# Optimization experiments

Measured on AMD Instinct MI355X. Metric: run time of the kernel, lower is better.

Reference implementation:

```python
import jax, jax.numpy as jnp
import numpy as np

THR = 0.5
IOU_THR = 0.2
K = 4096          # fixed pre-NMS candidate budget (jit-compatible stand-in for thr filtering + full sort)
FEAT_OFF = 5      # cols: 0 obj score, 1:5 box (l,t,r,b), 5: class-feature embedding


def setup_inputs() -> dict:
    key = jax.random.key(0)
    kx, kl, kt, kw, kh, ks, kp, kr = jax.random.split(key, 8)
    C, H, W = 261, 320, 320  # 5 + 256 feature channels
    x = jax.random.normal(kx, (1, C, H, W), dtype=jnp.float32)
    # plausible (l,t,r,b) boxes in padded-image coordinates so NMS has real work
    l = jax.random.uniform(kl, (1, 1, H, W), dtype=jnp.float32) * 600.0
    t = jax.random.uniform(kt, (1, 1, H, W), dtype=jnp.float32) * 600.0
    r = l + jax.random.uniform(kw, (1, 1, H, W), dtype=jnp.float32) * 60.0
    b = t + jax.random.uniform(kh, (1, 1, H, W), dtype=jnp.float32) * 60.0
    x = x.at[:, 1:5].set(jnp.concatenate([l, t, r, b], axis=1))
    state_matrix = jax.random.normal(ks, (16, 256), dtype=jnp.float32)
    padding = jax.random.uniform(kp, (2,), dtype=jnp.float32) * 10.0
    ratio = jax.random.uniform(kr, (1,), dtype=jnp.float32) * 0.6 + 0.4
    return {"x": x, "state_matrix": state_matrix, "padding": padding,
            "ratio": ratio, "image_width": 1280, "image_height": 768}


def _pairwise_iou(boxes, eps=1e-10):
    # boxes: [K, 4] as (l, t, r, b); returns [K, K]
    l, t, r, b = boxes[:, 0], boxes[:, 1], boxes[:, 2], boxes[:, 3]
    area = (r - l) * (b - t)
    iw = jnp.clip(jnp.minimum(r[:, None], r[None, :]) - jnp.maximum(l[:, None], l[None, :]), 0.0)
    ih = jnp.clip(jnp.minimum(b[:, None], b[None, :]) - jnp.maximum(t[:, None], t[None, :]), 0.0)
    inter = iw * ih
    union = area[:, None] + area[None, :] - inter + eps
    return inter / union


def reference(x, state_matrix, padding, ratio, image_width, image_height):
    B, C, H, W = x.shape
    out = x[0].reshape(C, H * W).T                      # [N, C]
    sig = jax.nn.sigmoid(out[:, 0])                     # sigmoid on objectness channel
    cls_logits = out[:, FEAT_OFF:] @ state_matrix.T     # [N, 16] class-state matmul
    cls_val = jnp.max(cls_logits, axis=1)
    cls_idx = jnp.argmax(cls_logits, axis=1)
    score = sig * cls_val                               # out[:,0] * cls_values
    valid = sig > THR                                   # out[0] > thr filter
    score = jnp.where(valid, score, -jnp.inf)
    topv, topi = jax.lax.top_k(score, K)                # descending sort, fixed budget
    boxes = out[topi, 1:5]                              # [K, 4] (l,t,r,b)
    cls_k = cls_idx[topi]
    area = (boxes[:, 2] - boxes[:, 0]) * (boxes[:, 3] - boxes[:, 1])
    iou = _pairwise_iou(boxes)                          # [K, K]

    alive0 = jnp.isfinite(topv)                         # only thr-passing candidates enter the queue
    kept0 = jnp.zeros((K,), dtype=bool)

    def body(carry, i):
        alive, kept = carry
        is_cur = alive[i]                               # still in the queue (not suppressed earlier)
        alive = alive.at[i].set(False)                  # pop top
        ious_i = iou[i]
        n_over = jnp.sum((ious_i >= IOU_THR) & alive)   # remaining boxes with iou >= thr
        accept = is_cur & (area[i] >= 4.0) & (n_over >= 10)
        kept = kept.at[i].set(accept)
        alive = jnp.where(accept, alive & (ious_i < IOU_THR), alive)  # suppress only on accept
        return (alive, kept), None

    (_, kept), _ = jax.lax.scan(body, (alive0, kept0), jnp.arange(K))

    keep = kept & (topv >= THR)                         # p[0,0] < thr -> skip
    inv_r = 1.0 / ratio[0]
    x1 = jnp.maximum((boxes[:, 0] - padding[0]) * inv_r, 0.0)
    y1 = jnp.maximum((boxes[:, 1] - padding[1]) * inv_r, 0.0)
    x2 = jnp.minimum((boxes[:, 2] - padding[0]) * inv_r, jnp.float32(image_width))
    y2 = jnp.minimum((boxes[:, 3] - padding[1]) * inv_r, jnp.float32(image_height))
    keep = keep & (x1 < image_width) & (y1 < image_height)

    dets = jnp.stack([jnp.ones((K,), jnp.float32), topv, x1, y1, x2, y2,
                      cls_k.astype(jnp.float32)], axis=1)   # [K, 7]
    dets = jnp.where(keep[:, None], dets, 0.0)
    return dets
```

## Files before the change

kernel.cpp:

```cpp
#include <hip/hip_runtime.h>
#include <hip/hip_bf16.h>
#include <math.h>

#define HW 102400
#define KSEL 4096
#define CAP 16384

__device__ inline unsigned fkey(float f) {
    unsigned u = __float_as_uint(f);
    return (u & 0x80000000u) ? ~u : (u | 0x80000000u);
}

__device__ inline unsigned wave_sum64_s(unsigned x) {
    x += (unsigned)__builtin_amdgcn_update_dpp(0, (int)x, 0x111, 0xf, 0xf, false);
    x += (unsigned)__builtin_amdgcn_update_dpp(0, (int)x, 0x112, 0xf, 0xf, false);
    x += (unsigned)__builtin_amdgcn_update_dpp(0, (int)x, 0x114, 0xf, 0xf, false);
    x += (unsigned)__builtin_amdgcn_update_dpp(0, (int)x, 0x118, 0xf, 0xf, false);
    x += (unsigned)__builtin_amdgcn_update_dpp(0, (int)x, 0x142, 0xa, 0xf, false);
    x += (unsigned)__builtin_amdgcn_update_dpp(0, (int)x, 0x143, 0xc, 0xf, false);
    return (unsigned)__builtin_amdgcn_readlane((int)x, 63);
}

__device__ inline unsigned long long readlane64(unsigned long long v, int l) {
    unsigned lo = (unsigned)__builtin_amdgcn_readlane((int)(unsigned)(v & 0xffffffffull), l);
    unsigned hi = (unsigned)__builtin_amdgcn_readlane((int)(unsigned)(v >> 32), l);
    return ((unsigned long long)hi << 32) | lo;
}

__global__ __launch_bounds__(256) void k_score(const float* __restrict__ x,
                                               const float* __restrict__ sm,
                                               float* __restrict__ score,
                                               int* __restrict__ clsidx) {
    __shared__ float swt[256][16];
    __shared__ float tile[2][16][256];
    int t = threadIdx.x;
    for (int i = t; i < 4096; i += 256) {
        int k = i >> 8, c = i & 255;
        swt[c][k] = sm[i];
    }
    int wave = t >> 6, lane = t & 63;
    size_t pxb = (size_t)blockIdx.x * 256;
    const float* xc = x + (size_t)5 * HW + pxb;

    float acc[16];
#pragma unroll
    for (int k = 0; k < 16; ++k) acc[k] = 0.f;

    float4 sa[4], sb[4];

#define LOADX(dst, ti)                                                         \
    _Pragma("unroll") for (int j = 0; j < 4; ++j)                              \
        dst[j] = *(const float4*)(xc + (size_t)((ti) * 16 + wave * 4 + j) * HW + lane * 4);
#define STOREX(src, s)                                                         \
    _Pragma("unroll") for (int j = 0; j < 4; ++j)                              \
        ((float4*)&tile[s][wave * 4 + j][0])[lane] = src[j];
#define COMP(s, ti)                                                            \
    _Pragma("unroll") for (int cc = 0; cc < 16; ++cc) {                        \
        float xv = tile[s][cc][t];                                             \
        const float4* w4 = (const float4*)&swt[(ti) * 16 + cc][0];             \
        float4 w0 = w4[0], w1 = w4[1], w2 = w4[2], w3 = w4[3];                 \
        acc[0]  = fmaf(xv, w0.x, acc[0]);  acc[1]  = fmaf(xv, w0.y, acc[1]);   \
        acc[2]  = fmaf(xv, w0.z, acc[2]);  acc[3]  = fmaf(xv, w0.w, acc[3]);   \
        acc[4]  = fmaf(xv, w1.x, acc[4]);  acc[5]  = fmaf(xv, w1.y, acc[5]);   \
        acc[6]  = fmaf(xv, w1.z, acc[6]);  acc[7]  = fmaf(xv, w1.w, acc[7]);   \
        acc[8]  = fmaf(xv, w2.x, acc[8]);  acc[9]  = fmaf(xv, w2.y, acc[9]);   \
        acc[10] = fmaf(xv, w2.z, acc[10]); acc[11] = fmaf(xv, w2.w, acc[11]);  \
        acc[12] = fmaf(xv, w3.x, acc[12]); acc[13] = fmaf(xv, w3.y, acc[13]);  \
        acc[14] = fmaf(xv, w3.z, acc[14]); acc[15] = fmaf(xv, w3.w, acc[15]);  \
    }

    LOADX(sa, 0);
    STOREX(sa, 0);
    LOADX(sa, 1);
    LOADX(sb, 2);
    __syncthreads();

#pragma unroll
    for (int k = 0; k < 16; k += 2) {
        COMP(k & 1, k);
        STOREX(sa, (k + 1) & 1);
        if (k + 3 < 16) LOADX(sa, k + 3);
        __syncthreads();
        COMP((k + 1) & 1, k + 1);
        if (k + 2 < 16) { STOREX(sb, k & 1); }
        if (k + 4 < 16) LOADX(sb, k + 4);
        __syncthreads();
    }
#undef LOADX
#undef STOREX
#undef COMP

    float mv = acc[0]; int mi = 0;
#pragma unroll
    for (int k = 1; k < 16; ++k)
        if (acc[k] > mv) { mv = acc[k]; mi = k; }
    int n = (int)pxb + t;
    float x0 = x[n];
    float sig = 1.0f / (1.0f + expf(-x0));
    float sc = (sig > 0.5f) ? sig * mv : -INFINITY;
    score[n] = sc;
    clsidx[n] = mi;
}

__global__ void k_hist(const float* __restrict__ score, unsigned* __restrict__ hist) {
    int n = blockIdx.x * 256 + threadIdx.x;
    float sc = score[n];
    if (sc != -INFINITY) atomicAdd(&hist[fkey(sc) >> 16], 1u);
}

__global__ __launch_bounds__(1024) void k_findp(const unsigned* __restrict__ hist,
                                                unsigned* __restrict__ meta) {
    __shared__ unsigned part[1024];
    __shared__ unsigned sgrp, s_after;
    __shared__ unsigned bins[64];
    int t = threadIdx.x;
    if (t == 0) { sgrp = 0; s_after = 0; }
    unsigned s = 0;
    const unsigned* hp = hist + t * 64;
    for (int i = 0; i < 64; ++i) s += hp[i];
    part[t] = s;
    __syncthreads();
    for (int off = 1; off < 1024; off <<= 1) {
        unsigned v = (t + off < 1024) ? part[t + off] : 0u;
        __syncthreads();
        part[t] += v;
        __syncthreads();
    }
    if (part[t] >= KSEL && (t == 1023 || part[t + 1] < KSEL)) {
        sgrp = (unsigned)t;
        s_after = (t == 1023) ? 0u : part[t + 1];
    }
    __syncthreads();
    unsigned g = sgrp, SA = s_after;
    if (t < 64) bins[t] = hist[g * 64 + t];
    __syncthreads();
    if (t == 0) {
        unsigned acc = SA, p = g * 64;
        for (int b = 63; b >= 0; --b) {
            acc += bins[b];
            if (acc >= KSEL) { p = g * 64 + (unsigned)b; break; }
        }
        meta[1] = p;
    }
}

__global__ void k_collect(const float* __restrict__ score,
                          unsigned* __restrict__ meta,
                          unsigned long long* __restrict__ cand) {
    int n = blockIdx.x * 256 + threadIdx.x;
    unsigned key = fkey(score[n]);
    if ((key >> 16) >= meta[1]) {
        unsigned pos = atomicAdd(&meta[0], 1u);
        if (pos < CAP)
            cand[pos] = ((unsigned long long)key << 32) | (unsigned)(~(unsigned)n);
    }
}

__global__ __launch_bounds__(256) void k_rank(const unsigned long long* __restrict__ cand,
                                              const unsigned* __restrict__ meta,
                                              const float* __restrict__ x,
                                              const float* __restrict__ score,
                                              const int* __restrict__ clsidx,
                                              float* __restrict__ topv,
                                              float* __restrict__ bl, float* __restrict__ bt,
                                              float* __restrict__ br, float* __restrict__ bb,
                                              float* __restrict__ area, int* __restrict__ clsk) {
    __shared__ unsigned long long tile[1024];
    int C = (int)meta[0]; if (C > CAP) C = CAP;
    int j = blockIdx.x * 256 + threadIdx.x;
    unsigned long long kj = (j < C) ? cand[j] : 0ull;
    unsigned rank = 0;
    for (int tb = 0; tb < C; tb += 1024) {
        int cnt = min(1024, C - tb);
        __syncthreads();
        for (int u = threadIdx.x; u < cnt; u += 256) tile[u] = cand[tb + u];
        __syncthreads();
        if (j < C)
            for (int u = 0; u < cnt; ++u) rank += (tile[u] > kj) ? 1u : 0u;
    }
    if (j < C && rank < KSEL) {
        unsigned n = ~(unsigned)(kj & 0xFFFFFFFFull);
        float l  = x[(size_t)1 * HW + n];
        float tt = x[(size_t)2 * HW + n];
        float r  = x[(size_t)3 * HW + n];
        float b  = x[(size_t)4 * HW + n];
        topv[rank] = score[n];
        bl[rank] = l; bt[rank] = tt; br[rank] = r; bb[rank] = b;
        area[rank] = (r - l) * (b - tt);
        clsk[rank] = clsidx[n];
    }
}

__global__ __launch_bounds__(256) void k_mask(const float* __restrict__ bl, const float* __restrict__ bt,
                                              const float* __restrict__ br, const float* __restrict__ bb,
                                              const float* __restrict__ area,
                                              unsigned long long* __restrict__ mask) {
    __shared__ float sl[256], st[256], sr[256], sb[256], sa[256];
    int t = threadIdx.x;
    int ic = blockIdx.x >> 4;
    int jc = blockIdx.x & 15;
    int i = ic * 256 + t;
    int j0 = jc * 256;
    sl[t] = bl[j0 + t]; st[t] = bt[j0 + t]; sr[t] = br[j0 + t];
    sb[t] = bb[j0 + t]; sa[t] = area[j0 + t];
    __syncthreads();
    float li = bl[i], ti = bt[i], ri = br[i], bi = bb[i], ai = area[i];
#pragma unroll
    for (int w = 0; w < 4; ++w) {
        unsigned long long m = 0;
        for (int k2 = 0; k2 < 64; ++k2) {
            int j = w * 64 + k2;
            float iw = fminf(ri, sr[j]) - fmaxf(li, sl[j]); iw = fmaxf(iw, 0.f);
            float ih = fminf(bi, sb[j]) - fmaxf(ti, st[j]); ih = fmaxf(ih, 0.f);
            float inter = iw * ih;
            float uni = ai + sa[j] - inter + 1e-10f;
            if (inter / uni >= 0.2f) m |= (1ull << k2);
        }
        mask[(size_t)i * 64 + (jc * 4 + w)] = m;
    }
}

__global__ __launch_bounds__(64, 1) void k_nms(const unsigned long long* __restrict__ mask,
                                               const float* __restrict__ topv,
                                               const float* __restrict__ area,
                                               unsigned long long* __restrict__ keptW) {
    __shared__ unsigned long long rowsL[2][4096];
    int lane = threadIdx.x;

#define STAGE(bb, s)                                                            \
    do {                                                                        \
        _Pragma("unroll") for (int q = 0; q < 32; ++q) {                        \
            int r_ = (bb) * 64 + q * 2 + (lane >> 5);                           \
            int P_ = (lane & 31) ^ (r_ & 31);                                   \
            const unsigned long long* gp_ = mask + (size_t)r_ * 64 + P_ * 2;    \
            __builtin_amdgcn_global_load_lds(                                   \
                (const __attribute__((address_space(1))) void*)gp_,             \
                (__attribute__((address_space(3))) void*)&rowsL[s][q * 128],    \
                16, 0, 0);                                                      \
        }                                                                       \
    } while (0)

    STAGE(0, 0);
    STAGE(1, 1);

    unsigned long long alive = 0, areaok = 0;
    for (int k = 0; k < 64; ++k) {
        float tv = topv[(size_t)k * 64 + lane];
        float ar = area[(size_t)k * 64 + lane];
        unsigned long long b1 = __ballot(tv != -INFINITY);
        unsigned long long b2 = __ballot(ar >= 4.0f);
        if (lane == k) { alive = b1; areaok = b2; }
    }

    for (int b = 0; b < 64; ++b) {
        if (b < 63) {
            asm volatile("s_waitcnt vmcnt(32)" ::: "memory");
        } else {
            asm volatile("s_waitcnt vmcnt(0)" ::: "memory");
        }
        __builtin_amdgcn_sched_barrier(0);

        const unsigned long long* rb = rowsL[b & 1];
        unsigned long long aw0snap = readlane64(alive, b);
        unsigned long long areaok0 = readlane64(areaok, b);

        int sw = lane & 31;
        unsigned cnt = 0;
#pragma unroll
        for (int P = 0; P < 32; ++P) {
            const ulonglong2 rv = *(const ulonglong2*)&rb[lane * 64 + ((P ^ sw) << 1)];
            unsigned long long a0 = readlane64(alive, 2 * P);
            unsigned long long a1 = readlane64(alive, 2 * P + 1);
            cnt += (unsigned)__popcll(rv.x & a0) + (unsigned)__popcll(rv.y & a1);
        }
        unsigned long long m_w0 = rb[lane * 64 + ((((b >> 1) ^ sw)) << 1) + (b & 1)];
        unsigned long long pfx = (lane == 63) ? ~0ull : ((1ull << (lane + 1)) - 1ull);
        cnt -= (unsigned)__popcll(m_w0 & aw0snap & pfx);

        bool candp = (cnt >= 10u) && ((areaok0 >> lane) & 1ull) && ((aw0snap >> lane) & 1ull);
        unsigned long long cand = __ballot(candp);
        unsigned long long keptB = 0;

        while (cand) {
            int j1 = __ffsll(cand) - 1;
            cand &= cand - 1;
            unsigned long long aw0cur = readlane64(alive, b);
            if (!((aw0cur >> j1) & 1ull)) continue;
            unsigned long long rw = rb[(size_t)j1 * 64 + (((lane >> 1) ^ (j1 & 31)) << 1) + (lane & 1)];
            unsigned long long awAdj = alive;
            unsigned long long pm = (j1 == 63) ? ~0ull : ((1ull << (j1 + 1)) - 1ull);
            if (lane == b) awAdj &= ~pm;
            unsigned c = (unsigned)__popcll(rw & awAdj);
            unsigned tt = wave_sum64_s(c);
            if (tt >= 10u) {
                alive &= ~rw;
                keptB |= 1ull << j1;
            }
        }

        if (lane == b) alive = 0;
        if (lane == 0) keptW[b] = keptB;

        if (b + 2 < 64) { STAGE(b + 2, (b & 1)); }
    }
#undef STAGE
}

__global__ __launch_bounds__(256) void k_out(const unsigned long long* __restrict__ keptW,
                                             const float* __restrict__ topv,
                                             const float* __restrict__ bl, const float* __restrict__ bt,
                                             const float* __restrict__ br, const float* __restrict__ bb,
                                             const int* __restrict__ clsk,
                                             const float* __restrict__ padding,
                                             const float* __restrict__ ratio,
                                             const int* __restrict__ piw, const int* __restrict__ pih,
                                             float* __restrict__ out) {
    int i = blockIdx.x * 256 + threadIdx.x;
    if (i >= KSEL) return;
    bool kept = (keptW[i >> 6] >> (i & 63)) & 1ull;
    float tv = topv[i];
    bool keep = kept && (tv >= 0.5f);
    float p0 = padding[0], p1 = padding[1];
    float invr = 1.0f / ratio[0];
    float W_ = (float)piw[0], H_ = (float)pih[0];
    float x1 = fmaxf((bl[i] - p0) * invr, 0.f);
    float y1 = fmaxf((bt[i] - p1) * invr, 0.f);
    float x2 = fminf((br[i] - p0) * invr, W_);
    float y2 = fminf((bb[i] - p1) * invr, H_);
    keep = keep && (x1 < W_) && (y1 < H_);
    float* o = out + (size_t)i * 7;
    if (keep) {
        o[0] = 1.0f; o[1] = tv; o[2] = x1; o[3] = y1; o[4] = x2; o[5] = y2;
        o[6] = (float)clsk[i];
    } else {
        o[0] = 0.f; o[1] = 0.f; o[2] = 0.f; o[3] = 0.f; o[4] = 0.f; o[5] = 0.f; o[6] = 0.f;
    }
}

extern "C" void kernel_launch(void* const* d_in, const int* in_sizes, int n_in,
                              void* d_out, int out_size, void* d_ws, size_t ws_size,
                              hipStream_t stream) {
    const float* x       = (const float*)d_in[0];
    const float* sm      = (const float*)d_in[1];
    const float* padding = (const float*)d_in[2];
    const float* ratio   = (const float*)d_in[3];
    const int*   piw     = (const int*)d_in[4];
    const int*   pih     = (const int*)d_in[5];
    float* out = (float*)d_out;
    char* ws = (char*)d_ws;

    float* score               = (float*)(ws + 0);
    int*   clsidx              = (int*)(ws + 409600);
    unsigned* hist             = (unsigned*)(ws + 819200);
    unsigned* meta             = (unsigned*)(ws + 1081344);
    unsigned long long* cand   = (unsigned long long*)(ws + 1081856);
    float* topv                = (float*)(ws + 1212928);
    float* bl                  = (float*)(ws + 1229312);
    float* bt                  = (float*)(ws + 1245696);
    float* br                  = (float*)(ws + 1262080);
    float* bb                  = (float*)(ws + 1278464);
    float* area                = (float*)(ws + 1294848);
    int*   clsk                = (int*)(ws + 1311232);
    unsigned long long* keptW  = (unsigned long long*)(ws + 1327616);
    unsigned long long* mask   = (unsigned long long*)(ws + 1328128);

    hipMemsetAsync(hist, 0, 262144 + 512, stream);

    k_score  <<<400, 256, 0, stream>>>(x, sm, score, clsidx);
    k_hist   <<<400, 256, 0, stream>>>(score, hist);
    k_findp  <<<1, 1024, 0, stream>>>(hist, meta);
    k_collect<<<400, 256, 0, stream>>>(score, meta, cand);
    k_rank   <<<CAP / 256, 256, 0, stream>>>(cand, meta, x, score, clsidx,
                                             topv, bl, bt, br, bb, area, clsk);
    k_mask   <<<256, 256, 0, stream>>>(bl, bt, br, bb, area, mask);
    k_nms    <<<1, 64, 0, stream>>>(mask, topv, area, keptW);
    k_out    <<<16, 256, 0, stream>>>(keptW, topv, bl, bt, br, bb, clsk,
                                      padding, ratio, piw, pih, out);
}
```

Measured before the change: 374.7 us.

## Split NMS block counting across four waves with LDS alive mask and batched verify

The serial NMS kernel goes from one wave to four. All four waves compute the per-row overlap counts in parallel: each row's 64 words are split over 4 threads, combined with DPP, and read against an alive mask broadcast through LDS. Wave 0 alone runs the sequential accept loop, preloading up to four candidate rows per iteration to hide LDS latency. Row staging moves to a rotated layout spread across waves. The price is three block barriers per 64-row block in a latency-bound single-block kernel.

```diff
diff --git a/kernel.cpp b/kernel.cpp
--- a/kernel.cpp
+++ b/kernel.cpp
@@ -220,22 +220,43 @@
     }
 }
 
-__global__ __launch_bounds__(64, 1) void k_nms(const unsigned long long* __restrict__ mask,
-                                               const float* __restrict__ topv,
-                                               const float* __restrict__ area,
-                                               unsigned long long* __restrict__ keptW) {
+__global__ __launch_bounds__(256, 1) void k_nms(const unsigned long long* __restrict__ mask,
+                                                const float* __restrict__ topv,
+                                                const float* __restrict__ area,
+                                                unsigned long long* __restrict__ keptW) {
     __shared__ unsigned long long rowsL[2][4096];
-    int lane = threadIdx.x;
+    __shared__ unsigned long long aliveL[64];
+    __shared__ unsigned cntL[64];
+    int t = threadIdx.x;
+    int lane = t & 63;
+    int W = t >> 6;
+    int g = t & 3;
+    int jrow = t >> 2;
+
+    unsigned long long alive = 0, areaok = 0, keptAcc = 0;
+    if (W == 0) {
+        for (int k = 0; k < 64; ++k) {
+            float tv = topv[(size_t)k * 64 + lane];
+            float ar = area[(size_t)k * 64 + lane];
+            unsigned long long b1 = __ballot(tv != -INFINITY);
+            unsigned long long b2 = __ballot(ar >= 4.0f);
+            if (lane == k) { alive = b1; areaok = b2; }
+        }
+        aliveL[lane] = alive;
+    }
 
 #define STAGE(bb, s)                                                            \
     do {                                                                        \
-        _Pragma("unroll") for (int q = 0; q < 32; ++q) {                        \
-            int r_ = (bb) * 64 + q * 2 + (lane >> 5);                           \
-            int P_ = (lane & 31) ^ (r_ & 31);                                   \
-            const unsigned long long* gp_ = mask + (size_t)r_ * 64 + P_ * 2;    \
+        _Pragma("unroll") for (int i = 0; i < 8; ++i) {                         \
+            int seg_ = i * 4 + W;                                               \
+            int r_ = seg_ * 2 + (lane >> 5);                                    \
+            int p_ = (lane & 31) * 2;                                           \
+            int wl_ = (p_ - 2 * r_) & 63;                                       \
+            const unsigned long long* gp_ =                                     \
+                mask + ((size_t)((bb) * 64 + r_) * 64 + wl_);                   \
             __builtin_amdgcn_global_load_lds(                                   \
                 (const __attribute__((address_space(1))) void*)gp_,             \
-                (__attribute__((address_space(3))) void*)&rowsL[s][q * 128],    \
+                (__attribute__((address_space(3))) void*)&rowsL[s][seg_ * 128], \
                 16, 0, 0);                                                      \
         }                                                                       \
     } while (0)
@@ -243,67 +264,82 @@
     STAGE(0, 0);
     STAGE(1, 1);
 
-    unsigned long long alive = 0, areaok = 0;
-    for (int k = 0; k < 64; ++k) {
-        float tv = topv[(size_t)k * 64 + lane];
-        float ar = area[(size_t)k * 64 + lane];
-        unsigned long long b1 = __ballot(tv != -INFINITY);
-        unsigned long long b2 = __ballot(ar >= 4.0f);
-        if (lane == k) { alive = b1; areaok = b2; }
+#define VER(jj, rw)                                                             \
+    {                                                                           \
+        unsigned long long awc = readlane64(alive, b);                          \
+        if ((awc >> (jj)) & 1ull) {                                             \
+            unsigned long long awAdj = alive;                                   \
+            unsigned long long pm = ((jj) == 63) ? ~0ull                        \
+                                                 : ((1ull << ((jj) + 1)) - 1ull); \
+            if (lane == b) awAdj &= ~pm;                                        \
+            unsigned c_ = (unsigned)__popcll((rw) & awAdj);                     \
+            unsigned tt_ = wave_sum64_s(c_);                                    \
+            if (tt_ >= 10u) { alive &= ~(rw); keptB |= 1ull << (jj); }          \
+        }                                                                       \
     }
 
     for (int b = 0; b < 64; ++b) {
-        if (b < 63) {
-            asm volatile("s_waitcnt vmcnt(32)" ::: "memory");
-        } else {
-            asm volatile("s_waitcnt vmcnt(0)" ::: "memory");
-        }
+        if (b < 63) asm volatile("s_waitcnt vmcnt(8)" ::: "memory");
+        else        asm volatile("s_waitcnt vmcnt(0)" ::: "memory");
         __builtin_amdgcn_sched_barrier(0);
-
-        const unsigned long long* rb = rowsL[b & 1];
-        unsigned long long aw0snap = readlane64(alive, b);
-        unsigned long long areaok0 = readlane64(areaok, b);
-
-        int sw = lane & 31;
+        __builtin_amdgcn_s_barrier();
+
+        const unsigned long long* rb = &rowsL[b & 1][0];
+
+        unsigned long long pfxj = (jrow == 63) ? ~0ull : ((1ull << (jrow + 1)) - 1ull);
+        int base_w = g * 16;
         unsigned cnt = 0;
 #pragma unroll
-        for (int P = 0; P < 32; ++P) {
-            const ulonglong2 rv = *(const ulonglong2*)&rb[lane * 64 + ((P ^ sw) << 1)];
-            unsigned long long a0 = readlane64(alive, 2 * P);
-            unsigned long long a1 = readlane64(alive, 2 * P + 1);
-            cnt += (unsigned)__popcll(rv.x & a0) + (unsigned)__popcll(rv.y & a1);
+        for (int q = 0; q < 8; ++q) {
+            int wl = base_w + q * 2;
+            int ph = (wl + 2 * jrow) & 63;
+            ulonglong2 rv = *(const ulonglong2*)&rb[jrow * 64 + ph];
+            ulonglong2 av = *(const ulonglong2*)&aliveL[wl];
+            unsigned cx = (unsigned)__popcll(rv.x & av.x);
+            unsigned cy = (unsigned)__popcll(rv.y & av.y);
+            cnt += cx + cy;
+            if (wl == b)     cnt -= (unsigned)__popcll(rv.x & av.x & pfxj);
+            if (wl + 1 == b) cnt -= (unsigned)__popcll(rv.y & av.y & pfxj);
         }
-        unsigned long long m_w0 = rb[lane * 64 + ((((b >> 1) ^ sw)) << 1) + (b & 1)];
-        unsigned long long pfx = (lane == 63) ? ~0ull : ((1ull << (lane + 1)) - 1ull);
-        cnt -= (unsigned)__popcll(m_w0 & aw0snap & pfx);
-
-        bool candp = (cnt >= 10u) && ((areaok0 >> lane) & 1ull) && ((aw0snap >> lane) & 1ull);
-        unsigned long long cand = __ballot(candp);
-        unsigned long long keptB = 0;
-
-        while (cand) {
-            int j1 = __ffsll(cand) - 1;
-            cand &= cand - 1;
-            unsigned long long aw0cur = readlane64(alive, b);
-            if (!((aw0cur >> j1) & 1ull)) continue;
-            unsigned long long rw = rb[(size_t)j1 * 64 + (((lane >> 1) ^ (j1 & 31)) << 1) + (lane & 1)];
-            unsigned long long awAdj = alive;
-            unsigned long long pm = (j1 == 63) ? ~0ull : ((1ull << (j1 + 1)) - 1ull);
-            if (lane == b) awAdj &= ~pm;
-            unsigned c = (unsigned)__popcll(rw & awAdj);
-            unsigned tt = wave_sum64_s(c);
-            if (tt >= 10u) {
-                alive &= ~rw;
-                keptB |= 1ull << j1;
+        cnt += (unsigned)__builtin_amdgcn_update_dpp(0, (int)cnt, 0xB1, 0xf, 0xf, false);
+        cnt += (unsigned)__builtin_amdgcn_update_dpp(0, (int)cnt, 0x4E, 0xf, 0xf, false);
+        if (g == 0) cntL[jrow] = cnt;
+        asm volatile("s_waitcnt lgkmcnt(0)" ::: "memory");
+        __builtin_amdgcn_s_barrier();
+
+        if (W == 0) {
+            unsigned long long keptB = 0;
+            unsigned long long aw0snap = readlane64(alive, b);
+            unsigned long long areaok0 = readlane64(areaok, b);
+            unsigned myc = cntL[lane];
+            bool candp = (myc >= 10u) && ((areaok0 >> lane) & 1ull) &&
+                         ((aw0snap >> lane) & 1ull);
+            unsigned long long cand = __ballot(candp);
+            while (cand) {
+                int j1 = __ffsll(cand) - 1; cand &= cand - 1;
+                int j2 = -1, j3 = -1, j4 = -1;
+                if (cand) { j2 = __ffsll(cand) - 1; cand &= cand - 1; }
+                if (cand) { j3 = __ffsll(cand) - 1; cand &= cand - 1; }
+                if (cand) { j4 = __ffsll(cand) - 1; cand &= cand - 1; }
+                unsigned long long r1 = rb[j1 * 64 + ((lane + 2 * j1) & 63)];
+                unsigned long long r2 = (j2 >= 0) ? rb[j2 * 64 + ((lane + 2 * j2) & 63)] : 0;
+                unsigned long long r3 = (j3 >= 0) ? rb[j3 * 64 + ((lane + 2 * j3) & 63)] : 0;
+                unsigned long long r4 = (j4 >= 0) ? rb[j4 * 64 + ((lane + 2 * j4) & 63)] : 0;
+                VER(j1, r1);
+                if (j2 >= 0) VER(j2, r2);
+                if (j3 >= 0) VER(j3, r3);
+                if (j4 >= 0) VER(j4, r4);
             }
+            if (lane == b) { alive = 0; keptAcc = keptB; }
+            aliveL[lane] = alive;
         }
-
-        if (lane == b) alive = 0;
-        if (lane == 0) keptW[b] = keptB;
-
-        if (b + 2 < 64) { STAGE(b + 2, (b & 1)); }
-    }
+        asm volatile("s_waitcnt lgkmcnt(0)" ::: "memory");
+        __builtin_amdgcn_s_barrier();
+        if (b + 2 < 64) STAGE(b + 2, b & 1);
+    }
+    if (W == 0) keptW[lane] = keptAcc;
 #undef STAGE
+#undef VER
 }
 
 __global__ __launch_bounds__(256) void k_out(const unsigned long long* __restrict__ keptW,
@@ -373,7 +409,7 @@
     k_rank   <<<CAP / 256, 256, 0, stream>>>(cand, meta, x, score, clsidx,
                                              topv, bl, bt, br, bb, area, clsk);
     k_mask   <<<256, 256, 0, stream>>>(bl, bt, br, bb, area, mask);
-    k_nms    <<<1, 64, 0, stream>>>(mask, topv, area, keptW);
+    k_nms    <<<1, 256, 0, stream>>>(mask, topv, area, keptW);
     k_out    <<<16, 256, 0, stream>>>(keptW, topv, bl, bt, br, bb, clsk,
                                       padding, ratio, piw, pih, out);
 }
```

New measurement: 324.7 us. 13.4% less time.
